# Kernel tuning notes

Measured on AMD Instinct MI355X. Metric: run time of the kernel, lower is better.

The kernel has to match this reference:

```python
import jax, jax.numpy as jnp
import numpy as np

BSZ, SEQ, DIM, NH = 2, 2048, 2048, 16
HD = DIM // NH  # 128


def setup_inputs() -> dict:
    key = jax.random.key(0)
    ks = jax.random.split(key, 6)
    x = jax.random.normal(ks[0], (BSZ, SEQ, DIM), dtype=jnp.float32)
    # torch Linear weights: [out_features, in_features]
    scale = 1.0 / np.sqrt(DIM)
    wq = jax.random.normal(ks[1], (DIM, DIM), dtype=jnp.float32) * scale
    wk = jax.random.normal(ks[2], (DIM, DIM), dtype=jnp.float32) * scale
    wv = jax.random.normal(ks[3], (DIM, DIM), dtype=jnp.float32) * scale
    wo = jax.random.normal(ks[4], (DIM, DIM), dtype=jnp.float32) * scale
    # RoPE freqs (llama style): theta=10000
    inv_freq = 1.0 / (10000.0 ** (jnp.arange(0, HD, 2, dtype=jnp.float32) / HD))  # [HD//2]
    t = jnp.arange(SEQ, dtype=jnp.float32)
    angles = jnp.outer(t, inv_freq)  # [SEQ, HD//2]
    freqs_cos = jnp.cos(angles)
    freqs_sin = jnp.sin(angles)
    # causal additive mask [SEQ, SEQ]
    mask = jnp.where(jnp.tril(jnp.ones((SEQ, SEQ), dtype=bool)), 0.0, -jnp.inf).astype(jnp.float32)
    return {"x": x, "wq": wq, "wk": wk, "wv": wv, "wo": wo,
            "freqs_cos": freqs_cos, "freqs_sin": freqs_sin, "mask": mask}


def _apply_rope(v, cos, sin):
    # v: [b, s, h, hd]; complex pairs are interleaved (even=real, odd=imag)
    b, s, h, hd = v.shape
    vr = v.reshape(b, s, h, hd // 2, 2)
    v0, v1 = vr[..., 0], vr[..., 1]
    c = cos[None, :, None, :]  # [1, s, 1, hd//2]
    sn = sin[None, :, None, :]
    out = jnp.stack([v0 * c - v1 * sn, v0 * sn + v1 * c], axis=-1)
    return out.reshape(b, s, h, hd)


def reference(x, wq, wk, wv, wo, freqs_cos, freqs_sin, mask):
    b, s, _ = x.shape
    xq = (x @ wq.T).reshape(b, s, NH, HD)
    xk = (x @ wk.T).reshape(b, s, NH, HD)
    xv = (x @ wv.T).reshape(b, s, NH, HD)
    xq = _apply_rope(xq, freqs_cos, freqs_sin)
    xk = _apply_rope(xk, freqs_cos, freqs_sin)
    # [b, h, s, s]
    scores = jnp.einsum('bqhd,bkhd->bhqk', xq, xk) / jnp.sqrt(jnp.float32(HD))
    scores = scores + mask[None, None, :, :]
    probs = jax.nn.softmax(scores.astype(jnp.float32), axis=-1).astype(scores.dtype)
    out = jnp.einsum('bhqk,bkhd->bqhd', probs, xv).reshape(b, s, NH * HD)
    return out @ wo.T
```

## Files before the change

### kernel.cpp

```cpp
#include <hip/hip_runtime.h>
#include <hip/hip_bf16.h>
#include <stdint.h>

typedef __bf16 bf16x8 __attribute__((ext_vector_type(8)));
typedef float f32x4 __attribute__((ext_vector_type(4)));
typedef unsigned short u16;
typedef unsigned int u32;

#define DEVI __device__ __forceinline__

DEVI u16 f2b(float f){ __bf16 h = (__bf16)f; return __builtin_bit_cast(u16, h); }
DEVI float b2f(u16 u){ return (float)__builtin_bit_cast(__bf16, u); }

constexpr int BSZ = 2, SEQ = 2048, DIM = 2048, NH = 16, HD = 128;

#if defined(__has_builtin)
#if __has_builtin(__builtin_amdgcn_global_load_lds)
#define HAVE_ASYNC_LDS 1
#endif
#endif

DEVI void cp16(void* lds, const void* g){
#ifdef HAVE_ASYNC_LDS
  auto gp = (const __attribute__((address_space(1))) u32*)(uintptr_t)g;
  auto lp = (__attribute__((address_space(3))) u32*)(uintptr_t)lds;
  __builtin_amdgcn_global_load_lds(gp, lp, 16, 0, 0);
#else
  *(uint4*)lds = *(const uint4*)g;
#endif
}

__global__ __launch_bounds__(256) void k_convert(
    const float* __restrict__ x, const float* __restrict__ wq,
    const float* __restrict__ wk, const float* __restrict__ wv,
    const float* __restrict__ wo,
    u16* __restrict__ xb, u16* __restrict__ wqkv, u16* __restrict__ wob)
{
  int e = (blockIdx.x * 256 + threadIdx.x) * 4;
  float4 v; u16* dp;
  if (e < 8388608){
    v = *(const float4*)&x[e]; dp = &xb[e];
  } else if (e < 20971520){
    int o = e - 8388608; int sec = o >> 22; int oo = o & 4194303;
    const float* w = (sec == 0) ? wq : ((sec == 1) ? wk : wv);
    v = *(const float4*)&w[oo]; dp = &wqkv[o];
  } else {
    int o = e - 20971520;
    v = *(const float4*)&wo[o]; dp = &wob[o];
  }
  ushort4 r; r.x = f2b(v.x); r.y = f2b(v.y); r.z = f2b(v.z); r.w = f2b(v.w);
  *(ushort4*)dp = r;
}

__global__ __launch_bounds__(256) void k_gemm_qkv(
    const u16* __restrict__ A, const u16* __restrict__ W,
    const float* __restrict__ fc, const float* __restrict__ fs,
    u16* __restrict__ Qd, u16* __restrict__ Kd, u16* __restrict__ Vd)
{
  __shared__ u16 As[128*32];
  __shared__ u16 Bs[128*32];
  __shared__ u16 Cs[128*136];
  const int t = threadIdx.x;
  const int lane = t & 63;
  const int l15 = lane & 15, quad = lane >> 4;
  const int wave = t >> 6;
  const int wr = (wave >> 1) * 64, wc = (wave & 1) * 64;
  const int tm = blockIdx.y * 128, tn = blockIdx.x * 128;
  const int arow = t >> 2, acol = (t & 3) * 8;

  f32x4 acc[4][4] = {};
  for (int k0 = 0; k0 < DIM; k0 += 32){
    __syncthreads();
    #pragma unroll
    for (int is = 0; is < 2; ++is){
      int row = is*64 + arow;
      cp16(&As[is*2048 + t*8], &A[(size_t)(tm + row)*DIM + k0 + acol]);
      cp16(&Bs[is*2048 + t*8], &W[(size_t)(tn + row)*DIM + k0 + acol]);
    }
    __syncthreads();
    bf16x8 af[4], bfr[4];
    #pragma unroll
    for (int i = 0; i < 4; ++i){
      af[i]  = *(const bf16x8*)&As[(wr + i*16 + l15)*32 + quad*8];
      bfr[i] = *(const bf16x8*)&Bs[(wc + i*16 + l15)*32 + quad*8];
    }
    #pragma unroll
    for (int mt = 0; mt < 4; ++mt)
      #pragma unroll
      for (int nt = 0; nt < 4; ++nt)
        acc[mt][nt] = __builtin_amdgcn_mfma_f32_16x16x32_bf16(af[mt], bfr[nt], acc[mt][nt], 0, 0, 0);
  }
  #pragma unroll
  for (int mt = 0; mt < 4; ++mt)
    #pragma unroll
    for (int nt = 0; nt < 4; ++nt)
      #pragma unroll
      for (int r = 0; r < 4; ++r)
        Cs[(wr + mt*16 + quad*4 + r)*136 + wc + nt*16 + l15] = f2b(acc[mt][nt][r]);
  __syncthreads();

  const int sec = tn >> 11;
  const int hh = (tn & 2047) >> 7;
  u16* dst = (sec == 0) ? Qd : ((sec == 1) ? Kd : Vd);
  const float qs = (sec == 0) ? (0.08838834764831845f * 1.4426950408889634f) : 1.0f;
  const int col0 = (t & 15) * 8;
  #pragma unroll
  for (int jj = 0; jj < 8; ++jj){
    int row = (t >> 4) + jj*16;
    int m = tm + row;
    int b = m >> 11, s = m & 2047;
    uint4 cv = *(const uint4*)&Cs[row*136 + col0];
    const u16* cp = (const u16*)&cv;
    u16 op[8];
    if (sec < 2){
      float4 c4 = *(const float4*)&fc[(size_t)s*64 + (col0 >> 1)];
      float4 s4 = *(const float4*)&fs[(size_t)s*64 + (col0 >> 1)];
      float cc[4] = {c4.x*qs, c4.y*qs, c4.z*qs, c4.w*qs};
      float ss[4] = {s4.x*qs, s4.y*qs, s4.z*qs, s4.w*qs};
      #pragma unroll
      for (int p = 0; p < 4; ++p){
        float a = b2f(cp[2*p]), bb = b2f(cp[2*p+1]);
        op[2*p]   = f2b(a*cc[p] - bb*ss[p]);
        op[2*p+1] = f2b(a*ss[p] + bb*cc[p]);
      }
    } else {
      #pragma unroll
      for (int p = 0; p < 8; ++p) op[p] = cp[p];
    }
    *(uint4*)&dst[((size_t)(b*NH + hh)*SEQ + s)*HD + col0] = *(const uint4*)op;
  }
}

__global__ __launch_bounds__(256) void k_vtrans(
    const u16* __restrict__ V, u16* __restrict__ Vt)
{
  __shared__ u16 ts[64*72];
  const int t = threadIdx.x;
  const int st = blockIdx.x, dt = blockIdx.y, bh = blockIdx.z;
  const size_t base  = (size_t)bh * SEQ * HD;
  const size_t baseT = (size_t)bh * HD * SEQ;
  #pragma unroll
  for (int i = 0; i < 2; ++i){
    int s = i*32 + (t>>3), c = t&7;
    *(uint4*)&ts[s*72 + c*8] = *(const uint4*)&V[base + (size_t)(st*64 + s)*HD + dt*64 + c*8];
  }
  __syncthreads();
  #pragma unroll
  for (int i = 0; i < 2; ++i){
    int d = i*32 + (t>>3), sc = t&7;
    u16 tmp[8];
    #pragma unroll
    for (int j = 0; j < 8; ++j) tmp[j] = ts[(sc*8 + j)*72 + d];
    *(uint4*)&Vt[baseT + (size_t)(dt*64 + d)*SEQ + st*64 + sc*8] = *(const uint4*)tmp;
  }
}

__global__ __launch_bounds__(256) void k_flash(
    const u16* __restrict__ Qd, const u16* __restrict__ Kd,
    const u16* __restrict__ Vt, u16* __restrict__ OP0, u16* __restrict__ OP1,
    float* __restrict__ Mp, float* __restrict__ Lp)
{
  __shared__ u16 Ks[64*144];
  __shared__ u16 Vs[128*72];
  __shared__ u16 Ps[4*32*72];

  const int t = threadIdx.x, lane = t & 63, wave = t >> 6;
  const int l15 = lane & 15, quad = lane >> 4;
  const int j = blockIdx.x >> 1, split = blockIdx.x & 1;
  const int h = blockIdx.y, b = blockIdx.z, bh = b*NH + h;
  const size_t base  = (size_t)bh * SEQ * HD;
  const size_t baseT = (size_t)bh * HD * SEQ;
  u16* Psw = &Ps[wave*32*72];
  u16* OPs = split ? OP1 : OP0;
  const int lo = 17*split, hi = lo + 17;
  const int qt0 = j, qt1 = 15 - j;
  const int len0 = 2*qt0 + 2;

  const int krow = t >> 4, kcol = (t & 15) * 8;
  const int vrow = t >> 3, vcol = (t & 7) * 8;

  for (int pass = 0; pass < 2; ++pass){
    const int qt = pass ? qt1 : qt0;
    const int len = 2*qt + 2;
    int kt0 = pass ? (lo - len0) : lo; if (kt0 < 0) kt0 = 0;
    int kt1 = pass ? (hi - len0) : hi; if (kt1 > len) kt1 = len;
    const int qb = qt*128 + wave*32;

    bf16x8 qf[2][4];
    #pragma unroll
    for (int mt = 0; mt < 2; ++mt)
      #pragma unroll
      for (int ks = 0; ks < 4; ++ks)
        qf[mt][ks] = *(const bf16x8*)&Qd[base + (size_t)(qb + mt*16 + l15)*HD + ks*32 + quad*8];

    f32x4 oacc[8][2] = {};
    float m_s[2] = {-1e30f, -1e30f}, l_s[2] = {0.f, 0.f};

    if (kt0 < kt1){
      uint4 kreg[4], vreg[4];
      #pragma unroll
      for (int i = 0; i < 4; ++i){
        kreg[i] = *(const uint4*)&Kd[base + (size_t)(kt0*64 + i*16 + krow)*HD + kcol];
        vreg[i] = *(const uint4*)&Vt[baseT + (size_t)(i*32 + vrow)*SEQ + kt0*64 + vcol];
      }
      for (int kt = kt0; kt < kt1; ++kt){
        __syncthreads();
        #pragma unroll
        for (int i = 0; i < 4; ++i){
          *(uint4*)&Ks[(i*16 + krow)*144 + kcol] = kreg[i];
          *(uint4*)&Vs[(i*32 + vrow)*72 + vcol] = vreg[i];
        }
        __syncthreads();
        if (kt + 1 < kt1){
          #pragma unroll
          for (int i = 0; i < 4; ++i){
            kreg[i] = *(const uint4*)&Kd[base + (size_t)((kt+1)*64 + i*16 + krow)*HD + kcol];
            vreg[i] = *(const uint4*)&Vt[baseT + (size_t)(i*32 + vrow)*SEQ + (kt+1)*64 + vcol];
          }
        }
        if (kt*64 <= qb + 31){
          f32x4 sacc[4][2] = {};
          #pragma unroll
          for (int ks = 0; ks < 4; ++ks){
            bf16x8 kf[4];
            #pragma unroll
            for (int nk = 0; nk < 4; ++nk)
              kf[nk] = *(const bf16x8*)&Ks[(nk*16 + l15)*144 + ks*32 + quad*8];
            #pragma unroll
            for (int nk = 0; nk < 4; ++nk)
              #pragma unroll
              for (int mt = 0; mt < 2; ++mt)
                sacc[nk][mt] = __builtin_amdgcn_mfma_f32_16x16x32_bf16(kf[nk], qf[mt][ks], sacc[nk][mt], 0, 0, 0);
          }
          #pragma unroll
          for (int nk = 0; nk < 4; ++nk)
            #pragma unroll
            for (int mt = 0; mt < 2; ++mt){
              int q = qb + mt*16 + l15;
              #pragma unroll
              for (int r = 0; r < 4; ++r){
                int key = kt*64 + nk*16 + quad*4 + r;
                if (key > q) sacc[nk][mt][r] = -1e30f;
              }
            }
          #pragma unroll
          for (int mt = 0; mt < 2; ++mt){
            float rm = -1e30f;
            #pragma unroll
            for (int nk = 0; nk < 4; ++nk)
              #pragma unroll
              for (int r = 0; r < 4; ++r) rm = fmaxf(rm, sacc[nk][mt][r]);
            rm = fmaxf(rm, __shfl_xor(rm, 16));
            rm = fmaxf(rm, __shfl_xor(rm, 32));
            float mnew = fmaxf(m_s[mt], rm);
            float alpha = exp2f(m_s[mt] - mnew);
            m_s[mt] = mnew;
            float rs = 0.f;
            #pragma unroll
            for (int nk = 0; nk < 4; ++nk){
              u16 pk[4];
              #pragma unroll
              for (int r = 0; r < 4; ++r){
                float p = exp2f(sacc[nk][mt][r] - mnew);
                rs += p;
                pk[r] = f2b(p);
              }
              *(uint2*)&Psw[(mt*16 + l15)*72 + nk*16 + quad*4] = *(const uint2*)pk;
            }
            rs += __shfl_xor(rs, 16);
            rs += __shfl_xor(rs, 32);
            l_s[mt] = l_s[mt]*alpha + rs;
            #pragma unroll
            for (int db = 0; db < 8; ++db)
              #pragma unroll
              for (int r = 0; r < 4; ++r) oacc[db][mt][r] *= alpha;
          }
          #pragma unroll
          for (int k2 = 0; k2 < 2; ++k2){
            bf16x8 pf[2];
            #pragma unroll
            for (int mt = 0; mt < 2; ++mt)
              pf[mt] = *(const bf16x8*)&Psw[(mt*16 + l15)*72 + k2*32 + quad*8];
            #pragma unroll
            for (int db = 0; db < 8; ++db){
              bf16x8 vf = *(const bf16x8*)&Vs[(db*16 + l15)*72 + k2*32 + quad*8];
              #pragma unroll
              for (int mt = 0; mt < 2; ++mt)
                oacc[db][mt] = __builtin_amdgcn_mfma_f32_16x16x32_bf16(vf, pf[mt], oacc[db][mt], 0, 0, 0);
            }
          }
        }
      }
    }
    #pragma unroll
    for (int mt = 0; mt < 2; ++mt){
      int s = qb + mt*16 + l15;
      #pragma unroll
      for (int db = 0; db < 8; ++db){
        u16 ok[4];
        #pragma unroll
        for (int r = 0; r < 4; ++r) ok[r] = f2b(oacc[db][mt][r]);
        *(uint2*)&OPs[(((size_t)(b*SEQ + s))*NH + h)*HD + db*16 + quad*4] = *(const uint2*)ok;
      }
      if (quad == 0){
        size_t mi = ((size_t)split*BSZ*NH + bh)*SEQ + s;
        Mp[mi] = m_s[mt];
        Lp[mi] = l_s[mt];
      }
    }
  }
}

__global__ __launch_bounds__(256) void k_combine(
    u16* __restrict__ OP0, const u16* __restrict__ OP1,
    const float* __restrict__ Mp, const float* __restrict__ Lp)
{
  size_t flat = ((size_t)blockIdx.x*256 + threadIdx.x)*8;
  int h = (int)((flat >> 7) & 15);
  int s = (int)((flat >> 11) & 2047);
  int b = (int)(flat >> 22);
  size_t row = ((size_t)(b*NH + h))*SEQ + s;
  const size_t off1 = (size_t)BSZ*NH*SEQ;
  float m0 = Mp[row], l0 = Lp[row];
  float m1 = Mp[row + off1], l1 = Lp[row + off1];
  float m = fmaxf(m0, m1);
  float w0 = exp2f(m0 - m), w1 = exp2f(m1 - m);
  float inv = 1.0f / (w0*l0 + w1*l1);
  uint4 a = *(const uint4*)&OP0[flat];
  uint4 c = *(const uint4*)&OP1[flat];
  const u16* pa = (const u16*)&a;
  const u16* pc = (const u16*)&c;
  u16 o[8];
  #pragma unroll
  for (int i = 0; i < 8; ++i)
    o[i] = f2b((b2f(pa[i])*w0 + b2f(pc[i])*w1) * inv);
  *(uint4*)&OP0[flat] = *(const uint4*)o;
}

__global__ __launch_bounds__(256) void k_gemm_out(
    const u16* __restrict__ A, const u16* __restrict__ W, float* __restrict__ out)
{
  __shared__ u16 As[128*32];
  __shared__ u16 Bs[128*32];
  const int t = threadIdx.x;
  const int lane = t & 63;
  const int l15 = lane & 15, quad = lane >> 4;
  const int wave = t >> 6;
  const int wr = (wave >> 1) * 64, wc = (wave & 1) * 64;
  const int tm = blockIdx.y * 128, tn = blockIdx.x * 128;
  const int arow = t >> 2, acol = (t & 3) * 8;

  f32x4 acc[4][4] = {};
  for (int k0 = 0; k0 < DIM; k0 += 32){
    __syncthreads();
    #pragma unroll
    for (int is = 0; is < 2; ++is){
      int row = is*64 + arow;
      cp16(&As[is*2048 + t*8], &A[(size_t)(tm + row)*DIM + k0 + acol]);
      cp16(&Bs[is*2048 + t*8], &W[(size_t)(tn + row)*DIM + k0 + acol]);
    }
    __syncthreads();
    bf16x8 af[4], bfr[4];
    #pragma unroll
    for (int i = 0; i < 4; ++i){
      af[i]  = *(const bf16x8*)&As[(wr + i*16 + l15)*32 + quad*8];
      bfr[i] = *(const bf16x8*)&Bs[(wc + i*16 + l15)*32 + quad*8];
    }
    #pragma unroll
    for (int mt = 0; mt < 4; ++mt)
      #pragma unroll
      for (int nt = 0; nt < 4; ++nt)
        acc[mt][nt] = __builtin_amdgcn_mfma_f32_16x16x32_bf16(af[mt], bfr[nt], acc[mt][nt], 0, 0, 0);
  }
  #pragma unroll
  for (int mt = 0; mt < 4; ++mt)
    #pragma unroll
    for (int nt = 0; nt < 4; ++nt)
      #pragma unroll
      for (int r = 0; r < 4; ++r){
        int row = tm + wr + mt*16 + quad*4 + r;
        int col = tn + wc + nt*16 + l15;
        out[(size_t)row*DIM + col] = acc[mt][nt][r];
      }
}

extern "C" void kernel_launch(void* const* d_in, const int* in_sizes, int n_in,
                              void* d_out, int out_size, void* d_ws, size_t ws_size,
                              hipStream_t stream)
{
  const float* x  = (const float*)d_in[0];
  const float* wq = (const float*)d_in[1];
  const float* wk = (const float*)d_in[2];
  const float* wv = (const float*)d_in[3];
  const float* wo = (const float*)d_in[4];
  const float* fc = (const float*)d_in[5];
  const float* fs = (const float*)d_in[6];
  float* out = (float*)d_out;

  char* ws = (char*)d_ws;
  u16* xb   = (u16*)(ws);
  u16* wqkv = (u16*)(ws + 16777216);
  u16* wob  = (u16*)(ws + 41943040);
  u16* Qr   = (u16*)(ws + 50331648);
  u16* Kr   = (u16*)(ws + 67108864);
  u16* Vr   = (u16*)(ws + 83886080);
  u16* Ob   = (u16*)(ws + 100663296);
  u16* VtT  = xb;
  u16* OP1  = wqkv;
  float* Mp = (float*)(ws + 33554432);
  float* Lp = (float*)(ws + 34078720);

  k_convert <<<24576, 256, 0, stream>>>(x, wq, wk, wv, wo, xb, wqkv, wob);
  k_gemm_qkv<<<dim3(48, 32), 256, 0, stream>>>(xb, wqkv, fc, fs, Qr, Kr, Vr);
  k_vtrans  <<<dim3(32, 2, 32), 256, 0, stream>>>(Vr, VtT);
  k_flash   <<<dim3(16, NH, BSZ), 256, 0, stream>>>(Qr, Kr, VtT, Ob, OP1, Mp, Lp);
  k_combine <<<4096, 256, 0, stream>>>(Ob, OP1, Mp, Lp);
  k_gemm_out<<<dim3(16, 32), 256, 0, stream>>>(Ob, wob, out);
}
```

Before: 489.3 us.

## Use 8 waves of 16 query rows each in flash attention kernel

The flash attention block grows from 4 to 8 waves (512 threads). Each wave now owns 16 query rows instead of 32, and K/V tile loads are split across twice as many threads. The causal mask is applied only on diagonal tiles, and the max and sum reductions are rewritten as trees. This is meant to raise occupancy and latency hiding with only 512 blocks on the GPU, at the cost of less K/V fragment reuse per wave and more LDS reads per MFMA.

New measurement: 457.7 us. 1.07x faster.

```diff
diff --git a/kernel.cpp b/kernel.cpp
--- a/kernel.cpp
+++ b/kernel.cpp
@@ -155,14 +155,14 @@
   }
 }
 
-__global__ __launch_bounds__(256) void k_flash(
+__global__ __launch_bounds__(512) void k_flash(
     const u16* __restrict__ Qd, const u16* __restrict__ Kd,
     const u16* __restrict__ Vt, u16* __restrict__ OP0, u16* __restrict__ OP1,
     float* __restrict__ Mp, float* __restrict__ Lp)
 {
-  __shared__ u16 Ks[64*144];
+  __shared__ u16 Ks[64*136];
   __shared__ u16 Vs[128*72];
-  __shared__ u16 Ps[4*32*72];
+  __shared__ u16 Ps[8*16*72];
 
   const int t = threadIdx.x, lane = t & 63, wave = t >> 6;
   const int l15 = lane & 15, quad = lane >> 4;
@@ -170,7 +170,7 @@
   const int h = blockIdx.y, b = blockIdx.z, bh = b*NH + h;
   const size_t base  = (size_t)bh * SEQ * HD;
   const size_t baseT = (size_t)bh * HD * SEQ;
-  u16* Psw = &Ps[wave*32*72];
+  u16* Psw = &Ps[wave*16*72];
   u16* OPs = split ? OP1 : OP0;
   const int lo = 17*split, hi = lo + 17;
   const int qt0 = j, qt1 = 15 - j;
@@ -184,128 +184,115 @@
     const int len = 2*qt + 2;
     int kt0 = pass ? (lo - len0) : lo; if (kt0 < 0) kt0 = 0;
     int kt1 = pass ? (hi - len0) : hi; if (kt1 > len) kt1 = len;
-    const int qb = qt*128 + wave*32;
-
-    bf16x8 qf[2][4];
-    #pragma unroll
-    for (int mt = 0; mt < 2; ++mt)
-      #pragma unroll
-      for (int ks = 0; ks < 4; ++ks)
-        qf[mt][ks] = *(const bf16x8*)&Qd[base + (size_t)(qb + mt*16 + l15)*HD + ks*32 + quad*8];
-
-    f32x4 oacc[8][2] = {};
-    float m_s[2] = {-1e30f, -1e30f}, l_s[2] = {0.f, 0.f};
+    const int qb = qt*128 + wave*16;
+
+    bf16x8 qf[4];
+    #pragma unroll
+    for (int ks = 0; ks < 4; ++ks)
+      qf[ks] = *(const bf16x8*)&Qd[base + (size_t)(qb + l15)*HD + ks*32 + quad*8];
+
+    f32x4 oacc[8] = {};
+    float m_s = -1e30f, l_s = 0.f;
 
     if (kt0 < kt1){
-      uint4 kreg[4], vreg[4];
-      #pragma unroll
-      for (int i = 0; i < 4; ++i){
-        kreg[i] = *(const uint4*)&Kd[base + (size_t)(kt0*64 + i*16 + krow)*HD + kcol];
-        vreg[i] = *(const uint4*)&Vt[baseT + (size_t)(i*32 + vrow)*SEQ + kt0*64 + vcol];
+      uint4 kreg[2], vreg[2];
+      #pragma unroll
+      for (int i = 0; i < 2; ++i){
+        kreg[i] = *(const uint4*)&Kd[base + (size_t)(kt0*64 + i*32 + krow)*HD + kcol];
+        vreg[i] = *(const uint4*)&Vt[baseT + (size_t)(i*64 + vrow)*SEQ + kt0*64 + vcol];
       }
       for (int kt = kt0; kt < kt1; ++kt){
         __syncthreads();
         #pragma unroll
-        for (int i = 0; i < 4; ++i){
-          *(uint4*)&Ks[(i*16 + krow)*144 + kcol] = kreg[i];
-          *(uint4*)&Vs[(i*32 + vrow)*72 + vcol] = vreg[i];
+        for (int i = 0; i < 2; ++i){
+          *(uint4*)&Ks[(i*32 + krow)*136 + kcol] = kreg[i];
+          *(uint4*)&Vs[(i*64 + vrow)*72 + vcol] = vreg[i];
         }
         __syncthreads();
         if (kt + 1 < kt1){
           #pragma unroll
-          for (int i = 0; i < 4; ++i){
-            kreg[i] = *(const uint4*)&Kd[base + (size_t)((kt+1)*64 + i*16 + krow)*HD + kcol];
-            vreg[i] = *(const uint4*)&Vt[baseT + (size_t)(i*32 + vrow)*SEQ + (kt+1)*64 + vcol];
+          for (int i = 0; i < 2; ++i){
+            kreg[i] = *(const uint4*)&Kd[base + (size_t)((kt+1)*64 + i*32 + krow)*HD + kcol];
+            vreg[i] = *(const uint4*)&Vt[baseT + (size_t)(i*64 + vrow)*SEQ + (kt+1)*64 + vcol];
           }
         }
-        if (kt*64 <= qb + 31){
-          f32x4 sacc[4][2] = {};
+        if (kt*64 <= qb + 15){
+          f32x4 sacc[4] = {};
           #pragma unroll
           for (int ks = 0; ks < 4; ++ks){
             bf16x8 kf[4];
             #pragma unroll
             for (int nk = 0; nk < 4; ++nk)
-              kf[nk] = *(const bf16x8*)&Ks[(nk*16 + l15)*144 + ks*32 + quad*8];
+              kf[nk] = *(const bf16x8*)&Ks[(nk*16 + l15)*136 + ks*32 + quad*8];
+            #pragma unroll
+            for (int nk = 0; nk < 4; ++nk)
+              sacc[nk] = __builtin_amdgcn_mfma_f32_16x16x32_bf16(kf[nk], qf[ks], sacc[nk], 0, 0, 0);
+          }
+          if (kt*64 + 63 > qb){
+            int q = qb + l15;
             #pragma unroll
             for (int nk = 0; nk < 4; ++nk)
               #pragma unroll
-              for (int mt = 0; mt < 2; ++mt)
-                sacc[nk][mt] = __builtin_amdgcn_mfma_f32_16x16x32_bf16(kf[nk], qf[mt][ks], sacc[nk][mt], 0, 0, 0);
-          }
-          #pragma unroll
-          for (int nk = 0; nk < 4; ++nk)
-            #pragma unroll
-            for (int mt = 0; mt < 2; ++mt){
-              int q = qb + mt*16 + l15;
-              #pragma unroll
               for (int r = 0; r < 4; ++r){
                 int key = kt*64 + nk*16 + quad*4 + r;
-                if (key > q) sacc[nk][mt][r] = -1e30f;
+                if (key > q) sacc[nk][r] = -1e30f;
               }
-            }
-          #pragma unroll
-          for (int mt = 0; mt < 2; ++mt){
-            float rm = -1e30f;
+          }
+          float m4[4];
+          #pragma unroll
+          for (int nk = 0; nk < 4; ++nk)
+            m4[nk] = fmaxf(fmaxf(sacc[nk][0], sacc[nk][1]), fmaxf(sacc[nk][2], sacc[nk][3]));
+          float rm = fmaxf(fmaxf(m4[0], m4[1]), fmaxf(m4[2], m4[3]));
+          rm = fmaxf(rm, __shfl_xor(rm, 16));
+          rm = fmaxf(rm, __shfl_xor(rm, 32));
+          float mnew = fmaxf(m_s, rm);
+          float alpha = exp2f(m_s - mnew);
+          m_s = mnew;
+          float s4[4];
+          #pragma unroll
+          for (int nk = 0; nk < 4; ++nk){
+            u16 pk[4];
+            float p0 = exp2f(sacc[nk][0] - mnew);
+            float p1 = exp2f(sacc[nk][1] - mnew);
+            float p2 = exp2f(sacc[nk][2] - mnew);
+            float p3 = exp2f(sacc[nk][3] - mnew);
+            pk[0] = f2b(p0); pk[1] = f2b(p1); pk[2] = f2b(p2); pk[3] = f2b(p3);
+            s4[nk] = (p0 + p1) + (p2 + p3);
+            *(uint2*)&Psw[l15*72 + nk*16 + quad*4] = *(const uint2*)pk;
+          }
+          float rs = (s4[0] + s4[1]) + (s4[2] + s4[3]);
+          rs += __shfl_xor(rs, 16);
+          rs += __shfl_xor(rs, 32);
+          l_s = l_s*alpha + rs;
+          #pragma unroll
+          for (int db = 0; db < 8; ++db)
             #pragma unroll
-            for (int nk = 0; nk < 4; ++nk)
-              #pragma unroll
-              for (int r = 0; r < 4; ++r) rm = fmaxf(rm, sacc[nk][mt][r]);
-            rm = fmaxf(rm, __shfl_xor(rm, 16));
-            rm = fmaxf(rm, __shfl_xor(rm, 32));
-            float mnew = fmaxf(m_s[mt], rm);
-            float alpha = exp2f(m_s[mt] - mnew);
-            m_s[mt] = mnew;
-            float rs = 0.f;
-            #pragma unroll
-            for (int nk = 0; nk < 4; ++nk){
-              u16 pk[4];
-              #pragma unroll
-              for (int r = 0; r < 4; ++r){
-                float p = exp2f(sacc[nk][mt][r] - mnew);
-                rs += p;
-                pk[r] = f2b(p);
-              }
-              *(uint2*)&Psw[(mt*16 + l15)*72 + nk*16 + quad*4] = *(const uint2*)pk;
-            }
-            rs += __shfl_xor(rs, 16);
-            rs += __shfl_xor(rs, 32);
-            l_s[mt] = l_s[mt]*alpha + rs;
-            #pragma unroll
-            for (int db = 0; db < 8; ++db)
-              #pragma unroll
-              for (int r = 0; r < 4; ++r) oacc[db][mt][r] *= alpha;
-          }
+            for (int r = 0; r < 4; ++r) oacc[db][r] *= alpha;
           #pragma unroll
           for (int k2 = 0; k2 < 2; ++k2){
-            bf16x8 pf[2];
-            #pragma unroll
-            for (int mt = 0; mt < 2; ++mt)
-              pf[mt] = *(const bf16x8*)&Psw[(mt*16 + l15)*72 + k2*32 + quad*8];
+            bf16x8 pf = *(const bf16x8*)&Psw[l15*72 + k2*32 + quad*8];
             #pragma unroll
             for (int db = 0; db < 8; ++db){
               bf16x8 vf = *(const bf16x8*)&Vs[(db*16 + l15)*72 + k2*32 + quad*8];
-              #pragma unroll
-              for (int mt = 0; mt < 2; ++mt)
-                oacc[db][mt] = __builtin_amdgcn_mfma_f32_16x16x32_bf16(vf, pf[mt], oacc[db][mt], 0, 0, 0);
+              oacc[db] = __builtin_amdgcn_mfma_f32_16x16x32_bf16(vf, pf, oacc[db], 0, 0, 0);
             }
           }
         }
       }
     }
-    #pragma unroll
-    for (int mt = 0; mt < 2; ++mt){
-      int s = qb + mt*16 + l15;
+    {
+      int s = qb + l15;
       #pragma unroll
       for (int db = 0; db < 8; ++db){
         u16 ok[4];
         #pragma unroll
-        for (int r = 0; r < 4; ++r) ok[r] = f2b(oacc[db][mt][r]);
+        for (int r = 0; r < 4; ++r) ok[r] = f2b(oacc[db][r]);
         *(uint2*)&OPs[(((size_t)(b*SEQ + s))*NH + h)*HD + db*16 + quad*4] = *(const uint2*)ok;
       }
       if (quad == 0){
         size_t mi = ((size_t)split*BSZ*NH + bh)*SEQ + s;
-        Mp[mi] = m_s[mt];
-        Lp[mi] = l_s[mt];
+        Mp[mi] = m_s;
+        Lp[mi] = l_s;
       }
     }
   }
@@ -413,7 +400,7 @@
   k_convert <<<24576, 256, 0, stream>>>(x, wq, wk, wv, wo, xb, wqkv, wob);
   k_gemm_qkv<<<dim3(48, 32), 256, 0, stream>>>(xb, wqkv, fc, fs, Qr, Kr, Vr);
   k_vtrans  <<<dim3(32, 2, 32), 256, 0, stream>>>(Vr, VtT);
-  k_flash   <<<dim3(16, NH, BSZ), 256, 0, stream>>>(Qr, Kr, VtT, Ob, OP1, Mp, Lp);
+  k_flash   <<<dim3(16, NH, BSZ), 512, 0, stream>>>(Qr, Kr, VtT, Ob, OP1, Mp, Lp);
   k_combine <<<4096, 256, 0, stream>>>(Ob, OP1, Mp, Lp);
   k_gemm_out<<<dim3(16, 32), 256, 0, stream>>>(Ob, wob, out);
 }
```
